# Optimization experiments

Measured on AMD Instinct MI355X. Metric: run time of the kernel, lower is better.

## Reference

```python
import jax, jax.numpy as jnp
import numpy as np

B, C, W, H = 256, 1, 512, 512
D0, D1 = 64, 64            # input_dims: crop/resample target
LATENT = 1024
HIST = 8                   # transformer_history_size (also attention heads)
DEPTH = 4
HEADS = 8
DIM_HEAD = 64              # n_heads arg is used as dim_head
INNER = HEADS * DIM_HEAD   # 512
MLP = LATENT
NCLS = 1000
EPS = 1e-5
RESNET_GAIN = 2.0 ** 7     # 7 identity ResidualBlocks, each does x += x


def setup_inputs() -> dict:
    key = jax.random.key(0)
    ks = jax.random.split(key, 12)
    def rn(k, shape):
        return jax.random.normal(k, shape, jnp.float32) * 0.02
    return dict(
        x=jax.random.normal(ks[0], (B, C, W, H), jnp.float32),
        transformation=jax.random.uniform(ks[1], (B, 4), dtype=jnp.float32),
        history=jnp.zeros((HIST, B, LATENT), jnp.float32),
        w_img=rn(ks[2], (D0 * D1, LATENT)), b_img=jnp.zeros((LATENT,), jnp.float32),
        ln1_s=jnp.ones((DEPTH, LATENT), jnp.float32), ln1_b=jnp.zeros((DEPTH, LATENT), jnp.float32),
        w_qkv=rn(ks[3], (DEPTH, LATENT, 3 * INNER)),
        w_o=rn(ks[4], (DEPTH, INNER, LATENT)), b_o=jnp.zeros((DEPTH, LATENT), jnp.float32),
        ln2_s=jnp.ones((DEPTH, LATENT), jnp.float32), ln2_b=jnp.zeros((DEPTH, LATENT), jnp.float32),
        w_ff1=rn(ks[5], (DEPTH, LATENT, MLP)), b_ff1=jnp.zeros((DEPTH, MLP), jnp.float32),
        w_ff2=rn(ks[6], (DEPTH, MLP, LATENT)), b_ff2=jnp.zeros((DEPTH, LATENT), jnp.float32),
        w_cls=rn(ks[7], (HIST * LATENT, NCLS)), b_cls=jnp.zeros((NCLS,), jnp.float32),
        w_tr=rn(ks[8], (HIST * LATENT, 4)), b_tr=jnp.zeros((4,), jnp.float32),
    )


def _ln(x, s, b):
    m = x.mean(-1, keepdims=True)
    v = x.var(-1, keepdims=True)
    return (x - m) / jnp.sqrt(v + EPS) * s + b


def _crop_one(img, sc):
    # img [C,W,H], sc = [px, py, zx, zy]; nearest crop+resample to (D0, D1)
    px, py, zx, zy = sc[0], sc[1], sc[2], sc[3]
    x1 = px * (W - D0)
    y1 = py * (H - D1)
    xs = jnp.minimum(W - x1, zx * (W - D0) + D0)
    ys = jnp.minimum(H - y1, zy * (H - D1) + D1)
    xi = jnp.clip((jnp.floor(jnp.arange(D0, dtype=jnp.float32) / D0 * xs) + x1).astype(jnp.int32), 0, W - 1)
    yi = jnp.clip((jnp.floor(jnp.arange(D1, dtype=jnp.float32) / D1 * ys) + y1).astype(jnp.int32), 0, H - 1)
    # itertools.product(c, xi, yi) ordering == reshape(-1) of [C, D0, D1]
    return img[:, xi[:, None], yi[None, :]].reshape(-1)


def _forward(x, transformation, history, w_img, b_img, ln1_s, ln1_b, w_qkv, w_o, b_o,
             ln2_s, ln2_b, w_ff1, b_ff1, w_ff2, b_ff2, w_cls, b_cls, w_tr, b_tr):
    crops = jax.vmap(_crop_one)(x, transformation)          # [B, C*D0*D1]
    feats = crops * RESNET_GAIN                             # ResNet18 == scale by 2^7
    image_latent = feats @ w_img + b_img                    # [B, LATENT]
    # history.append(latent); take last HIST; stack dim=1 -> [B, HIST, LATENT]
    hist = jnp.transpose(history, (1, 0, 2))                # [B, HIST, LATENT]
    z = jnp.concatenate([hist[:, 1:], image_latent[:, None, :]], axis=1)
    scale = DIM_HEAD ** -0.5
    for i in range(DEPTH):
        h = _ln(z, ln1_s[i], ln1_b[i])
        qkv = h @ w_qkv[i]                                  # [B, HIST, 3*INNER]
        q, k, v = jnp.split(qkv, 3, axis=-1)
        q = q.reshape(B, HIST, HEADS, DIM_HEAD).transpose(0, 2, 1, 3)
        k = k.reshape(B, HIST, HEADS, DIM_HEAD).transpose(0, 2, 1, 3)
        v = v.reshape(B, HIST, HEADS, DIM_HEAD).transpose(0, 2, 1, 3)
        attn = jax.nn.softmax(jnp.einsum('bhid,bhjd->bhij', q, k) * scale, axis=-1)
        o = jnp.einsum('bhij,bhjd->bhid', attn, v).transpose(0, 2, 1, 3).reshape(B, HIST, INNER)
        z = o @ w_o[i] + b_o[i] + z
        h2 = _ln(z, ln2_s[i], ln2_b[i])
        z = jax.nn.gelu(h2 @ w_ff1[i] + b_ff1[i], approximate=False) @ w_ff2[i] + b_ff2[i] + z
    tl = z.reshape(B, HIST * LATENT)
    class_pred = tl @ w_cls + b_cls                         # [B, NCLS]
    transform_pred = jax.nn.sigmoid(tl @ w_tr + b_tr)       # [B, 4]
    return class_pred, transform_pred


def reference(x, transformation, history, w_img, b_img, ln1_s, ln1_b, w_qkv, w_o, b_o,
              ln2_s, ln2_b, w_ff1, b_ff1, w_ff2, b_ff2, w_cls, b_cls, w_tr, b_tr):
    return _forward(x, transformation, history, w_img, b_img, ln1_s, ln1_b, w_qkv, w_o, b_o,
                    ln2_s, ln2_b, w_ff1, b_ff1, w_ff2, b_ff2, w_cls, b_cls, w_tr, b_tr)
```

## Files before the change

kernel.cpp:

```cpp
#include <hip/hip_runtime.h>
#include <cstdint>
#include <cstddef>

typedef __attribute__((ext_vector_type(8))) __bf16 bf16x8;
typedef __attribute__((ext_vector_type(8))) unsigned short u16x8;
typedef __attribute__((ext_vector_type(4))) float f32x4;
typedef __attribute__((ext_vector_type(4))) unsigned short u16x4;

__device__ __forceinline__ unsigned short f2bf(float f) {
  unsigned int u = __builtin_bit_cast(unsigned int, f);
  u += 0x7fffu + ((u >> 16) & 1u);
  return (unsigned short)(u >> 16);
}
__device__ __forceinline__ float bf2f(unsigned short u) {
  return __builtin_bit_cast(float, ((unsigned int)u) << 16);
}

__device__ void wcast_tile(char* smemc, int bid,
    const float* s_img, const float* s_qkv, const float* s_o,
    const float* s_ff1, const float* s_ff2, const float* s_cls,
    unsigned short* d_img, unsigned short* d_qkv, unsigned short* d_o,
    unsigned short* d_ff1, unsigned short* d_ff2, unsigned short* d_cls) {
  float (*tile)[65] = (float (*)[65])smemc;
  const float* src; unsigned short* dst; int K, N, Npad, rel;
  if (bid < 1024)       { src = s_img; dst = d_img; K = 4096; N = 1024; Npad = 1024; rel = bid; }
  else if (bid < 2560)  { rel = bid - 1024; int l = rel / 384; rel -= l * 384;
                          src = s_qkv + (size_t)l * 1024 * 1536; dst = d_qkv + (size_t)l * 1536 * 1024;
                          K = 1024; N = 1536; Npad = 1536; }
  else if (bid < 3072)  { rel = bid - 2560; int l = rel / 128; rel -= l * 128;
                          src = s_o   + (size_t)l * 512 * 1024;  dst = d_o   + (size_t)l * 1024 * 512;
                          K = 512;  N = 1024; Npad = 1024; }
  else if (bid < 4096)  { rel = bid - 3072; int l = rel / 256; rel -= l * 256;
                          src = s_ff1 + (size_t)l * 1024 * 1024; dst = d_ff1 + (size_t)l * 1024 * 1024;
                          K = 1024; N = 1024; Npad = 1024; }
  else if (bid < 5120)  { rel = bid - 4096; int l = rel / 256; rel -= l * 256;
                          src = s_ff2 + (size_t)l * 1024 * 1024; dst = d_ff2 + (size_t)l * 1024 * 1024;
                          K = 1024; N = 1024; Npad = 1024; }
  else                  { rel = bid - 5120; src = s_cls; dst = d_cls; K = 8192; N = 1000; Npad = 1024; }
  int tilesX = Npad >> 6;
  int nx = rel % tilesX, ky = rel / tilesX;
  int n0 = nx << 6, k0 = ky << 6;
  int t = threadIdx.x;
#pragma unroll
  for (int i = 0; i < 4; ++i) {
    int slot = t + i * 256;
    int kk = slot >> 4, cq = slot & 15;
    int n = n0 + cq * 4;
    float4 v;
    if (n + 3 < N) v = *(const float4*)(src + (size_t)(k0 + kk) * N + n);
    else {
      v.x = v.y = v.z = v.w = 0.0f;
      if (n < N)     v.x = src[(size_t)(k0 + kk) * N + n];
      if (n + 1 < N) v.y = src[(size_t)(k0 + kk) * N + n + 1];
      if (n + 2 < N) v.z = src[(size_t)(k0 + kk) * N + n + 2];
      if (n + 3 < N) v.w = src[(size_t)(k0 + kk) * N + n + 3];
    }
    tile[kk][cq * 4 + 0] = v.x;
    tile[kk][cq * 4 + 1] = v.y;
    tile[kk][cq * 4 + 2] = v.z;
    tile[kk][cq * 4 + 3] = v.w;
  }
  __syncthreads();
#pragma unroll
  for (int i = 0; i < 4; ++i) {
    int slot = t + i * 256;
    int n = slot >> 4, kq = slot & 15;
    u16x4 o;
    o.x = f2bf(tile[kq * 4 + 0][n]);
    o.y = f2bf(tile[kq * 4 + 1][n]);
    o.z = f2bf(tile[kq * 4 + 2][n]);
    o.w = f2bf(tile[kq * 4 + 3][n]);
    *(u16x4*)(dst + (size_t)(n0 + n) * K + k0 + kq * 4) = o;
  }
}

template <int BK, int ITERS>
__device__ __forceinline__ void stage_tile(const unsigned short* __restrict__ g, int ld,
                                           int k0, char* lbase, int tid) {
  constexpr int CH = BK / 8;
#pragma unroll
  for (int it = 0; it < ITERS; ++it) {
    int c = tid + it * 256;
    int r = c / CH;
    int slot = c & (CH - 1);
    int gc = slot ^ (r & (CH - 1));
    const unsigned short* src = g + (size_t)r * ld + (k0 + gc * 8);
    char* dst = lbase + c * 16;
    __builtin_amdgcn_global_load_lds((__attribute__((address_space(1))) void*)src,
                                     (__attribute__((address_space(3))) void*)dst, 16, 0, 0);
  }
}

template <int BK>
__device__ __forceinline__ bf16x8 ld_frag(const char* base, int row, int k8) {
  constexpr int CH = BK / 8;
  int off = row * (BK * 2) + ((k8 ^ (row & (CH - 1))) << 4);
  return *(const bf16x8*)(base + off);
}

template <int TN, int ACT, int OMODE, bool RES, int BK>
__device__ void gemm_tile(char* smem,
    const unsigned short* __restrict__ A, int lda,
    const unsigned short* __restrict__ BT, int ldb, int Kloop,
    const float* __restrict__ bias, const unsigned short* __restrict__ res,
    float* __restrict__ outF, unsigned short* __restrict__ outB,
    int ldC, int Nstore, int m0, int n0, int koff) {
  constexpr int MR = (TN == 64) ? 2 : 4;
  constexpr int ABYTES = 128 * BK * 2;
  constexpr int BUFS = (128 + TN) * BK * 2;
  constexpr int AITERS = BK / 16;
  constexpr int BITERS = TN * BK / 2048;
  const int tid = threadIdx.x;
  const int lane = tid & 63;
  const int wid = tid >> 6;
  const int rowbase = (TN == 64) ? wid * 32 : (wid >> 1) * 64;
  const int colbase = (TN == 64) ? 0 : (wid & 1) * 64;
  const unsigned short* Ag = A + (size_t)m0 * lda + koff;
  const unsigned short* Bg = BT + (size_t)n0 * ldb + koff;
  f32x4 acc[MR][4];
#pragma unroll
  for (int m = 0; m < MR; m++)
#pragma unroll
    for (int n = 0; n < 4; n++) acc[m][n] = 0.f;
  const int nt = Kloop / BK;
  stage_tile<BK, AITERS>(Ag, lda, 0, smem, tid);
  stage_tile<BK, BITERS>(Bg, ldb, 0, smem + ABYTES, tid);
  __syncthreads();
  int cur = 0;
  const int rA = lane & 15, kq = lane >> 4;
  for (int t = 0; t < nt; ++t) {
    if (t + 1 < nt) {
      stage_tile<BK, AITERS>(Ag, lda, (t + 1) * BK, smem + (cur ^ 1) * BUFS, tid);
      stage_tile<BK, BITERS>(Bg, ldb, (t + 1) * BK, smem + (cur ^ 1) * BUFS + ABYTES, tid);
    }
    const char* la = smem + cur * BUFS;
    const char* lb = la + ABYTES;
#pragma unroll
    for (int kk = 0; kk < BK / 32; ++kk) {
      int k8 = kk * 4 + kq;
      bf16x8 af[MR], bfr[4];
#pragma unroll
      for (int m = 0; m < MR; m++) af[m] = ld_frag<BK>(la, rowbase + m * 16 + rA, k8);
#pragma unroll
      for (int n = 0; n < 4; n++) bfr[n] = ld_frag<BK>(lb, colbase + n * 16 + rA, k8);
#pragma unroll
      for (int m = 0; m < MR; m++)
#pragma unroll
        for (int n = 0; n < 4; n++)
          acc[m][n] = __builtin_amdgcn_mfma_f32_16x16x32_bf16(af[m], bfr[n], acc[m][n], 0, 0, 0);
    }
    __syncthreads();
    cur ^= 1;
  }
  const int rb = m0 + rowbase + (kq << 2);
  const int cb = n0 + colbase + rA;
#pragma unroll
  for (int m = 0; m < MR; m++)
#pragma unroll
    for (int n = 0; n < 4; n++) {
      int cg = cb + n * 16;
      if (cg >= Nstore) continue;
      float bv = bias ? bias[cg] : 0.0f;
#pragma unroll
      for (int j = 0; j < 4; j++) {
        int rg = rb + m * 16 + j;
        float v = acc[m][n][j] + bv;
        if (RES) v += bf2f(res[(size_t)rg * ldC + cg]);
        if (ACT == 1) v = 0.5f * v * (1.0f + erff(v * 0.70710678118654752f));
        if (OMODE == 0) {
          outF[(size_t)rg * ldC + cg] = v;
        } else {
          outB[(size_t)rg * ldC + cg] = f2bf(v);
        }
      }
    }
}

#define SLABW 200
__global__ __launch_bounds__(256) void qkvattn(
    const unsigned short* __restrict__ h,
    const unsigned short* __restrict__ BTq,
    unsigned short* __restrict__ obuf) {
  __shared__ __align__(16) char smem[65536];
  const int tid = threadIdx.x, lane = tid & 63, wid = tid >> 6;
  const int p = blockIdx.x;
  const int xslot = p & 7, rem = p >> 3;
  const int hh = rem & 7;
  const int my = xslot + 8 * (rem >> 3);
  const int m0 = my << 6;
  const int wr = wid >> 1, wc = wid & 1;
  const unsigned short* Ag = h + (size_t)m0 * 1024;
  const unsigned short* Bseg0 = BTq + (size_t)(hh * 64) * 1024;
  const unsigned short* Bseg1 = BTq + (size_t)(512 + hh * 64) * 1024;
  const unsigned short* Bseg2 = BTq + (size_t)(1024 + hh * 64) * 1024;
  constexpr int BUFS = 32768;
  f32x4 acc[2][6];
#pragma unroll
  for (int m = 0; m < 2; m++)
#pragma unroll
    for (int n = 0; n < 6; n++) acc[m][n] = 0.f;
  const int rA = lane & 15, kq = lane >> 4;
  stage_tile<64, 2>(Ag, 1024, 0, smem, tid);
  stage_tile<64, 2>(Bseg0, 1024, 0, smem + 8192, tid);
  stage_tile<64, 2>(Bseg1, 1024, 0, smem + 16384, tid);
  stage_tile<64, 2>(Bseg2, 1024, 0, smem + 24576, tid);
  __syncthreads();
  int cur = 0;
  for (int t = 0; t < 16; ++t) {
    if (t + 1 < 16) {
      char* nb = smem + (cur ^ 1) * BUFS;
      stage_tile<64, 2>(Ag, 1024, (t + 1) << 6, nb, tid);
      stage_tile<64, 2>(Bseg0, 1024, (t + 1) << 6, nb + 8192, tid);
      stage_tile<64, 2>(Bseg1, 1024, (t + 1) << 6, nb + 16384, tid);
      stage_tile<64, 2>(Bseg2, 1024, (t + 1) << 6, nb + 24576, tid);
    }
    const char* la = smem + cur * BUFS;
#pragma unroll
    for (int kk = 0; kk < 2; ++kk) {
      int k8 = kk * 4 + kq;
      bf16x8 af[2], bfr[6];
#pragma unroll
      for (int m = 0; m < 2; m++) af[m] = ld_frag<64>(la, wr * 32 + m * 16 + rA, k8);
#pragma unroll
      for (int n = 0; n < 6; n++) {
        int cidx = wc * 96 + n * 16 + rA;
        bfr[n] = ld_frag<64>(la + 8192 + (cidx >> 6) * 8192, cidx & 63, k8);
      }
#pragma unroll
      for (int m = 0; m < 2; m++)
#pragma unroll
        for (int n = 0; n < 6; n++)
          acc[m][n] = __builtin_amdgcn_mfma_f32_16x16x32_bf16(af[m], bfr[n], acc[m][n], 0, 0, 0);
    }
    __syncthreads();
    cur ^= 1;
  }
  unsigned short* slab = (unsigned short*)smem;
  float* Sb = (float*)(smem + 64 * SLABW * 2 + wid * 512);
#pragma unroll
  for (int m = 0; m < 2; m++)
#pragma unroll
    for (int n = 0; n < 6; n++) {
      int r = wr * 32 + m * 16 + (kq << 2);
      int c = wc * 96 + n * 16 + rA;
#pragma unroll
      for (int j = 0; j < 4; j++) slab[(size_t)(r + j) * SLABW + c] = f2bf(acc[m][n][j]);
    }
  __syncthreads();
  {
#pragma unroll
    for (int e = 0; e < 2; ++e) {
      int idx = e * 64 + lane;
      int bl = idx >> 6;
      int i = (idx >> 3) & 7, j = idx & 7;
      int rb8 = wid * 16 + bl * 8;
      const u16x8* qrow = (const u16x8*)(slab + (size_t)(rb8 + i) * SLABW);
      const u16x8* krow = (const u16x8*)(slab + (size_t)(rb8 + j) * SLABW + 64);
      float s = 0.f;
#pragma unroll
      for (int q8 = 0; q8 < 8; ++q8) {
        u16x8 qv = qrow[q8], kv = krow[q8];
#pragma unroll
        for (int u = 0; u < 8; ++u) s = fmaf(bf2f(qv[u]), bf2f(kv[u]), s);
      }
      Sb[bl * 64 + i * 8 + j] = s * 0.125f;
    }
    if (lane < 16) {
      float4 r0 = ((const float4*)(Sb + lane * 8))[0];
      float4 r1 = ((const float4*)(Sb + lane * 8))[1];
      float mx = fmaxf(fmaxf(fmaxf(r0.x, r0.y), fmaxf(r0.z, r0.w)),
                       fmaxf(fmaxf(r1.x, r1.y), fmaxf(r1.z, r1.w)));
      float e0 = expf(r0.x - mx), e1 = expf(r0.y - mx), e2 = expf(r0.z - mx), e3 = expf(r0.w - mx);
      float e4_ = expf(r1.x - mx), e5 = expf(r1.y - mx), e6 = expf(r1.z - mx), e7 = expf(r1.w - mx);
      float inv = 1.0f / (e0 + e1 + e2 + e3 + e4_ + e5 + e6 + e7);
      ((float4*)(Sb + lane * 8))[0] = make_float4(e0 * inv, e1 * inv, e2 * inv, e3 * inv);
      ((float4*)(Sb + lane * 8))[1] = make_float4(e4_ * inv, e5 * inv, e6 * inv, e7 * inv);
    }
#pragma unroll
    for (int bl = 0; bl < 2; ++bl) {
      int rb8 = wid * 16 + bl * 8;
      float vreg[8];
#pragma unroll
      for (int jj = 0; jj < 8; ++jj) vreg[jj] = bf2f(slab[(size_t)(rb8 + jj) * SLABW + 128 + lane]);
      int browg = (my * 8 + wid * 2 + bl) * 8;
#pragma unroll
      for (int i = 0; i < 8; ++i) {
        float4 p0 = ((const float4*)(Sb + (bl * 64 + i * 8)))[0];
        float4 p1 = ((const float4*)(Sb + (bl * 64 + i * 8)))[1];
        float o = p0.x * vreg[0] + p0.y * vreg[1] + p0.z * vreg[2] + p0.w * vreg[3] +
                  p1.x * vreg[4] + p1.y * vreg[5] + p1.z * vreg[6] + p1.w * vreg[7];
        obuf[(size_t)(browg + i) * 512 + hh * 64 + lane] = f2bf(o);
      }
    }
  }
}

__global__ __launch_bounds__(256) void front1(
    const float* __restrict__ x, const float* __restrict__ tr,
    const float* __restrict__ w_img, const float* __restrict__ w_qkv, const float* __restrict__ w_o,
    const float* __restrict__ w_ff1, const float* __restrict__ w_ff2, const float* __restrict__ w_cls,
    unsigned short* BT_img, unsigned short* BT_qkv, unsigned short* BT_o,
    unsigned short* BT_ff1, unsigned short* BT_ff2, unsigned short* BT_cls,
    unsigned short* feats) {
  __shared__ __align__(16) char smem[16640];
  int bid = blockIdx.x;
  int tid = threadIdx.x;
  if (bid < 1024) {
    wcast_tile(smem, bid, w_img, w_qkv, w_o, w_ff1, w_ff2, w_cls,
               BT_img, BT_qkv, BT_o, BT_ff1, BT_ff2, BT_cls);
  } else {
    int b = bid - 1024;
    int* xi = (int*)smem;
    int* yi = xi + 64;
    float px = tr[b * 4 + 0], py = tr[b * 4 + 1], zx = tr[b * 4 + 2], zy = tr[b * 4 + 3];
    float x1 = __fmul_rn(px, 448.0f);
    float y1 = __fmul_rn(py, 448.0f);
    float xs = fminf(__fsub_rn(512.0f, x1), __fadd_rn(__fmul_rn(zx, 448.0f), 64.0f));
    float ys = fminf(__fsub_rn(512.0f, y1), __fadd_rn(__fmul_rn(zy, 448.0f), 64.0f));
    if (tid < 64) {
      float u = __fmul_rn(__fmul_rn((float)tid, 0.015625f), xs);
      int v = (int)(__fadd_rn(floorf(u), x1));
      xi[tid] = min(max(v, 0), 511);
    } else if (tid < 128) {
      int tt = tid - 64;
      float u = __fmul_rn(__fmul_rn((float)tt, 0.015625f), ys);
      int v = (int)(__fadd_rn(floorf(u), y1));
      yi[tt] = min(max(v, 0), 511);
    }
    __syncthreads();
    const float* img = x + (size_t)b * 262144;
    for (int p = tid; p < 4096; p += 256) {
      int i = p >> 6, j = p & 63;
      float val = img[xi[i] * 512 + yi[j]] * 128.0f;
      feats[(size_t)b * 4096 + p] = f2bf(val);
    }
  }
}

__global__ __launch_bounds__(256) void k_img(
    const unsigned short* __restrict__ feats, const unsigned short* __restrict__ BT_img,
    float* __restrict__ part, const float* __restrict__ hist, unsigned short* __restrict__ z,
    const float* __restrict__ w_img, const float* __restrict__ w_qkv, const float* __restrict__ w_o,
    const float* __restrict__ w_ff1, const float* __restrict__ w_ff2, const float* __restrict__ w_cls,
    unsigned short* BT_img_d, unsigned short* BT_qkv, unsigned short* BT_o,
    unsigned short* BT_ff1, unsigned short* BT_ff2, unsigned short* BT_cls) {
  __shared__ __align__(16) char smem[49152];
  int bid = blockIdx.x;
  if (bid < 256) {
    int xslot = bid & 7, rem = bid >> 3;
    int nx = rem & 15, chi = rem >> 4;
    int c = xslot + 8 * chi;
    int sk = c >> 1, my = c & 1;
    gemm_tile<64, 0, 0, false, 64>(smem, feats, 4096, BT_img, 4096, 512,
                                   nullptr, nullptr, part + (size_t)sk * 262144, nullptr,
                                   1024, 1024, my * 128, nx * 64, sk * 512);
  } else if (bid < 6400) {
    wcast_tile(smem, 1024 + bid - 256, w_img, w_qkv, w_o, w_ff1, w_ff2, w_cls,
               BT_img_d, BT_qkv, BT_o, BT_ff1, BT_ff2, BT_cls);
  } else {
    int idx = (bid - 6400) * 256 + threadIdx.x;
    int off = idx * 4;
    int b = off / 7168;
    int r = off - b * 7168;
    int i = r >> 10, c = r & 1023;
    float4 v = *(const float4*)(hist + (size_t)(i + 1) * 262144 + (size_t)b * 1024 + c);
    u16x4 o;
    o.x = f2bf(v.x); o.y = f2bf(v.y); o.z = f2bf(v.z); o.w = f2bf(v.w);
    *(u16x4*)(z + (size_t)b * 8192 + i * 1024 + c) = o;
  }
}

__device__ __forceinline__ void ln_row(const unsigned short* __restrict__ z, int row,
                                       const float* __restrict__ sc, const float* __restrict__ bi,
                                       unsigned short* __restrict__ h) {
  int lane = threadIdx.x & 63;
  const unsigned short* zr = z + (size_t)row * 1024;
  float vf[16];
  float s = 0.f, q = 0.f;
#pragma unroll
  for (int i = 0; i < 2; i++) {
    u16x8 v = *(const u16x8*)(zr + lane * 8 + i * 512);
#pragma unroll
    for (int u = 0; u < 8; u++) {
      float f = bf2f(v[u]);
      vf[i * 8 + u] = f;
      s += f; q += f * f;
    }
  }
#pragma unroll
  for (int off = 32; off; off >>= 1) { s += __shfl_xor(s, off); q += __shfl_xor(q, off); }
  float mean = s * (1.0f / 1024.0f);
  float var = q * (1.0f / 1024.0f) - mean * mean;
  float rstd = rsqrtf(var + 1e-5f);
#pragma unroll
  for (int i = 0; i < 2; i++) {
    int c = lane * 8 + i * 512;
    float4 s0 = *(const float4*)(sc + c);
    float4 s1 = *(const float4*)(sc + c + 4);
    float4 b0 = *(const float4*)(bi + c);
    float4 b1 = *(const float4*)(bi + c + 4);
    u16x8 o;
    o[0] = f2bf((vf[i * 8 + 0] - mean) * rstd * s0.x + b0.x);
    o[1] = f2bf((vf[i * 8 + 1] - mean) * rstd * s0.y + b0.y);
    o[2] = f2bf((vf[i * 8 + 2] - mean) * rstd * s0.z + b0.z);
    o[3] = f2bf((vf[i * 8 + 3] - mean) * rstd * s0.w + b0.w);
    o[4] = f2bf((vf[i * 8 + 4] - mean) * rstd * s1.x + b1.x);
    o[5] = f2bf((vf[i * 8 + 5] - mean) * rstd * s1.y + b1.y);
    o[6] = f2bf((vf[i * 8 + 6] - mean) * rstd * s1.z + b1.z);
    o[7] = f2bf((vf[i * 8 + 7] - mean) * rstd * s1.w + b1.w);
    *(u16x8*)(h + (size_t)row * 1024 + c) = o;
  }
}

__global__ __launch_bounds__(256) void imgred_ln(
    const float* __restrict__ part, const float* __restrict__ b_img,
    unsigned short* __restrict__ z,
    const float* __restrict__ sc, const float* __restrict__ bi,
    unsigned short* __restrict__ h) {
  __shared__ float ws[8];
  int m = blockIdx.x, tid = threadIdx.x;
  int lane = tid & 63, wid = tid >> 6;
  int c = tid * 4;
  float4 a = {0.f, 0.f, 0.f, 0.f};
  for (int p = 0; p < 8; ++p) {
    float4 v = *(const float4*)(part + (size_t)p * 262144 + m * 1024 + c);
    a.x += v.x; a.y += v.y; a.z += v.z; a.w += v.w;
  }
  float4 bv = *(const float4*)(b_img + c);
  a.x += bv.x; a.y += bv.y; a.z += bv.z; a.w += bv.w;
  u16x4 zo;
  zo.x = f2bf(a.x); zo.y = f2bf(a.y); zo.z = f2bf(a.z); zo.w = f2bf(a.w);
  *(u16x4*)(z + (size_t)m * 8192 + 7168 + c) = zo;
  float s = a.x + a.y + a.z + a.w;
  float q = a.x * a.x + a.y * a.y + a.z * a.z + a.w * a.w;
#pragma unroll
  for (int off = 32; off; off >>= 1) { s += __shfl_xor(s, off); q += __shfl_xor(q, off); }
  if (lane == 0) { ws[wid * 2] = s; ws[wid * 2 + 1] = q; }
  __syncthreads();
  float S4 = ws[0] + ws[2] + ws[4] + ws[6];
  float Q4 = ws[1] + ws[3] + ws[5] + ws[7];
  float mean = S4 * (1.0f / 1024.0f);
  float var = Q4 * (1.0f / 1024.0f) - mean * mean;
  float rstd = rsqrtf(var + 1e-5f);
  float4 sv = *(const float4*)(sc + c);
  float4 bb = *(const float4*)(bi + c);
  u16x4 o;
  o.x = f2bf((a.x - mean) * rstd * sv.x + bb.x);
  o.y = f2bf((a.y - mean) * rstd * sv.y + bb.y);
  o.z = f2bf((a.z - mean) * rstd * sv.z + bb.z);
  o.w = f2bf((a.w - mean) * rstd * sv.w + bb.w);
  *(u16x4*)(h + (size_t)(m * 8 + 7) * 1024 + c) = o;
#pragma unroll
  for (int rr = 0; rr < 2; ++rr) {
    int r = wid * 2 + rr;
    if (r < 7) ln_row(z, m * 8 + r, sc, bi, h);
  }
}

__global__ __launch_bounds__(256) void ln_kernel(const unsigned short* __restrict__ z,
                                                 const float* __restrict__ sc,
                                                 const float* __restrict__ bi,
                                                 unsigned short* __restrict__ h) {
  int row = blockIdx.x * 4 + (threadIdx.x >> 6);
  ln_row(z, row, sc, bi, h);
}

template <int TN, int ACT, int OMODE, bool RES, int BK>
__global__ __launch_bounds__(256) void gemm_k(
    const unsigned short* __restrict__ A, int lda,
    const unsigned short* __restrict__ BT, int ldb, int Kloop,
    const float* __restrict__ bias, const unsigned short* __restrict__ res,
    float* __restrict__ outF, unsigned short* __restrict__ outB,
    int ldC, int Nstore) {
  constexpr int BUFS = (128 + TN) * BK * 2;
  __shared__ __align__(16) char smem[2 * BUFS];
  int p = blockIdx.x;
  int xslot = p & 7, rem = p >> 3;
  int nx = rem & 15;
  int my = xslot + 8 * (rem >> 4);
  gemm_tile<TN, ACT, OMODE, RES, BK>(smem, A, lda, BT, ldb, Kloop, bias, res, outF, outB,
                                     ldC, Nstore, my * 128, nx * TN, 0);
}

__global__ __launch_bounds__(256) void k_cls(
    const unsigned short* __restrict__ z, const unsigned short* __restrict__ BT_cls,
    float* __restrict__ part, const float* __restrict__ w_tr,
    const float* __restrict__ b_tr, float* __restrict__ outF) {
  __shared__ __align__(16) char smem[49152];
  int bid = blockIdx.x;
  int tid = threadIdx.x;
  if (bid < 256) {
    int xslot = bid & 7, rem = bid >> 3;
    int nx = rem & 15, chi = rem >> 4;
    int c = xslot + 8 * chi;
    int sk = c >> 1, my = c & 1;
    gemm_tile<64, 0, 0, false, 64>(smem, z, 8192, BT_cls, 8192, 1024,
                                   nullptr, nullptr, part + (size_t)sk * 262144, nullptr,
                                   1024, 1024, my * 128, nx * 64, sk * 1024);
  } else {
    int m = bid - 256;
    const unsigned short* row = z + (size_t)m * 8192;
    float a0 = 0.f, a1 = 0.f, a2 = 0.f, a3 = 0.f;
    for (int k = tid; k < 8192; k += 256) {
      float xv = bf2f(row[k]);
      const float* wr = w_tr + (size_t)k * 4;
      a0 += xv * wr[0]; a1 += xv * wr[1]; a2 += xv * wr[2]; a3 += xv * wr[3];
    }
    float (*red)[4] = (float (*)[4])smem;
    red[tid][0] = a0; red[tid][1] = a1; red[tid][2] = a2; red[tid][3] = a3;
    __syncthreads();
    for (int s = 128; s > 0; s >>= 1) {
      if (tid < s) {
#pragma unroll
        for (int o = 0; o < 4; o++) red[tid][o] += red[tid + s][o];
      }
      __syncthreads();
    }
    if (tid < 4) {
      float v = red[0][tid] + b_tr[tid];
      outF[256000 + m * 4 + tid] = 1.0f / (1.0f + expf(-v));
    }
  }
}

__global__ __launch_bounds__(256) void clsred(const float* __restrict__ part,
                                              const float* __restrict__ b_cls,
                                              float* __restrict__ outF) {
  int m = blockIdx.x, c = threadIdx.x * 4;
  float4 a = {0.f, 0.f, 0.f, 0.f};
  for (int p = 0; p < 8; ++p) {
    float4 v = *(const float4*)(part + (size_t)p * 262144 + m * 1024 + c);
    a.x += v.x; a.y += v.y; a.z += v.z; a.w += v.w;
  }
  if (c >= 1000) return;
  float* drow = outF + (size_t)m * 1000;
  float vals[4] = {a.x, a.y, a.z, a.w};
  if (c + 3 < 1000) {
    *(float4*)(drow + c) = make_float4(vals[0] + b_cls[c], vals[1] + b_cls[c + 1],
                                       vals[2] + b_cls[c + 2], vals[3] + b_cls[c + 3]);
  } else {
    for (int j = 0; j < 4 && c + j < 1000; ++j) drow[c + j] = vals[j] + b_cls[c + j];
  }
}

extern "C" void kernel_launch(void* const* d_in, const int* in_sizes, int n_in,
                              void* d_out, int out_size, void* d_ws, size_t ws_size,
                              hipStream_t stream) {
  const float* x      = (const float*)d_in[0];
  const float* tr     = (const float*)d_in[1];
  const float* hist   = (const float*)d_in[2];
  const float* w_img  = (const float*)d_in[3];
  const float* b_img  = (const float*)d_in[4];
  const float* ln1_s  = (const float*)d_in[5];
  const float* ln1_b  = (const float*)d_in[6];
  const float* w_qkv  = (const float*)d_in[7];
  const float* w_o    = (const float*)d_in[8];
  const float* b_o    = (const float*)d_in[9];
  const float* ln2_s  = (const float*)d_in[10];
  const float* ln2_b  = (const float*)d_in[11];
  const float* w_ff1  = (const float*)d_in[12];
  const float* b_ff1  = (const float*)d_in[13];
  const float* w_ff2  = (const float*)d_in[14];
  const float* b_ff2  = (const float*)d_in[15];
  const float* w_cls  = (const float*)d_in[16];
  const float* b_cls  = (const float*)d_in[17];
  const float* w_tr   = (const float*)d_in[18];
  const float* b_tr   = (const float*)d_in[19];
  float* outF = (float*)d_out;

  char* w = (char*)d_ws;
  auto alloc = [&](size_t bytes) { char* p = w; w += (bytes + 255) & ~(size_t)255; return p; };
  unsigned short* BT_img = (unsigned short*)alloc((size_t)1024 * 4096 * 2);
  unsigned short* BT_qkv = (unsigned short*)alloc((size_t)4 * 1536 * 1024 * 2);
  unsigned short* BT_o   = (unsigned short*)alloc((size_t)4 * 1024 * 512 * 2);
  unsigned short* BT_ff1 = (unsigned short*)alloc((size_t)4 * 1024 * 1024 * 2);
  unsigned short* BT_ff2 = (unsigned short*)alloc((size_t)4 * 1024 * 1024 * 2);
  unsigned short* BT_cls = (unsigned short*)alloc((size_t)1024 * 8192 * 2);
  unsigned short* feats  = (unsigned short*)alloc((size_t)256 * 4096 * 2);
  unsigned short* z      = (unsigned short*)alloc((size_t)2048 * 1024 * 2);
  unsigned short* h      = (unsigned short*)alloc((size_t)2048 * 1024 * 2);
  unsigned short* obuf   = (unsigned short*)alloc((size_t)2048 * 512 * 2);
  unsigned short* g      = (unsigned short*)alloc((size_t)2048 * 1024 * 2);
  float*          part   = (float*)alloc((size_t)8 * 256 * 1024 * 4);
  if ((size_t)(w - (char*)d_ws) > ws_size) return;

  front1<<<1280, 256, 0, stream>>>(x, tr, w_img, w_qkv, w_o, w_ff1, w_ff2, w_cls,
                                   BT_img, BT_qkv, BT_o, BT_ff1, BT_ff2, BT_cls, feats);
  k_img<<<8192, 256, 0, stream>>>(feats, BT_img, part, hist, z,
                                  w_img, w_qkv, w_o, w_ff1, w_ff2, w_cls,
                                  BT_img, BT_qkv, BT_o, BT_ff1, BT_ff2, BT_cls);
  imgred_ln<<<256, 256, 0, stream>>>(part, b_img, z, ln1_s, ln1_b, h);

  for (int i = 0; i < 4; ++i) {
    const unsigned short* Wq = BT_qkv + (size_t)i * 1536 * 1024;
    const unsigned short* Wo = BT_o   + (size_t)i * 1024 * 512;
    const unsigned short* W1 = BT_ff1 + (size_t)i * 1024 * 1024;
    const unsigned short* W2 = BT_ff2 + (size_t)i * 1024 * 1024;
    if (i > 0)
      ln_kernel<<<512, 256, 0, stream>>>(z, ln1_s + i * 1024, ln1_b + i * 1024, h);
    qkvattn<<<256, 256, 0, stream>>>(h, Wq, obuf);
    gemm_k<64, 0, 1, true, 64><<<256, 256, 0, stream>>>(
        obuf, 512, Wo, 512, 512, b_o + i * 1024, z, nullptr, z, 1024, 1024);
    ln_kernel<<<512, 256, 0, stream>>>(z, ln2_s + i * 1024, ln2_b + i * 1024, h);
    gemm_k<64, 1, 1, false, 64><<<256, 256, 0, stream>>>(
        h, 1024, W1, 1024, 1024, b_ff1 + i * 1024, nullptr, nullptr, g, 1024, 1024);
    gemm_k<64, 0, 1, true, 64><<<256, 256, 0, stream>>>(
        g, 1024, W2, 1024, 1024, b_ff2 + i * 1024, z, nullptr, z, 1024, 1024);
  }

  k_cls<<<512, 256, 0, stream>>>(z, BT_cls, part, w_tr, b_tr, outF);
  clsred<<<256, 256, 0, stream>>>(part, b_cls, outF);
}
```

Measured before the change: 323.1 us.

## Triple-buffer GEMM LDS staging with explicit vmcnt waits instead of full syncs

Converts the double-buffered async global-to-LDS pipeline in the shared GEMM tile and the fused QKV-attention kernel to a three-stage ring. Each iteration waits on vmcnt only until the oldest stage has landed and uses one raw barrier, where before it drained all loads with __syncthreads. Loads are issued two tiles ahead so memory latency can hide behind more MFMA work. In exchange LDS per block grows by half, which may reduce occupancy, and correctness depends on the hand-set vmcnt thresholds matching the number of issued loads.

```diff
diff --git a/kernel.cpp b/kernel.cpp
--- a/kernel.cpp
+++ b/kernel.cpp
@@ -14,6 +14,13 @@
 }
 __device__ __forceinline__ float bf2f(unsigned short u) {
   return __builtin_bit_cast(float, ((unsigned int)u) << 16);
+}
+
+template <int N> __device__ __forceinline__ void wait_vm() {
+  if constexpr (N == 0)      asm volatile("s_waitcnt vmcnt(0)" ::: "memory");
+  else if constexpr (N == 6) asm volatile("s_waitcnt vmcnt(6)" ::: "memory");
+  else if constexpr (N == 8) asm volatile("s_waitcnt vmcnt(8)" ::: "memory");
+  else                       asm volatile("s_waitcnt vmcnt(0)" ::: "memory");
 }
 
 __device__ void wcast_tile(char* smemc, int bid,
@@ -72,6 +79,7 @@
     o.w = f2bf(tile[kq * 4 + 3][n]);
     *(u16x4*)(dst + (size_t)(n0 + n) * K + k0 + kq * 4) = o;
   }
+  __syncthreads();
 }
 
 template <int BK, int ITERS>
@@ -110,6 +118,7 @@
   constexpr int BUFS = (128 + TN) * BK * 2;
   constexpr int AITERS = BK / 16;
   constexpr int BITERS = TN * BK / 2048;
+  constexpr int VM = AITERS + BITERS;
   const int tid = threadIdx.x;
   const int lane = tid & 63;
   const int wid = tid >> 6;
@@ -125,13 +134,17 @@
   const int nt = Kloop / BK;
   stage_tile<BK, AITERS>(Ag, lda, 0, smem, tid);
   stage_tile<BK, BITERS>(Bg, ldb, 0, smem + ABYTES, tid);
-  __syncthreads();
+  stage_tile<BK, AITERS>(Ag, lda, BK, smem + BUFS, tid);
+  stage_tile<BK, BITERS>(Bg, ldb, BK, smem + BUFS + ABYTES, tid);
   int cur = 0;
   const int rA = lane & 15, kq = lane >> 4;
   for (int t = 0; t < nt; ++t) {
-    if (t + 1 < nt) {
-      stage_tile<BK, AITERS>(Ag, lda, (t + 1) * BK, smem + (cur ^ 1) * BUFS, tid);
-      stage_tile<BK, BITERS>(Bg, ldb, (t + 1) * BK, smem + (cur ^ 1) * BUFS + ABYTES, tid);
+    if (t + 1 < nt) wait_vm<VM>(); else wait_vm<0>();
+    __builtin_amdgcn_s_barrier();
+    if (t + 2 < nt) {
+      int nb = cur + 2; if (nb >= 3) nb -= 3;
+      stage_tile<BK, AITERS>(Ag, lda, (t + 2) * BK, smem + nb * BUFS, tid);
+      stage_tile<BK, BITERS>(Bg, ldb, (t + 2) * BK, smem + nb * BUFS + ABYTES, tid);
     }
     const char* la = smem + cur * BUFS;
     const char* lb = la + ABYTES;
@@ -149,8 +162,7 @@
         for (int n = 0; n < 4; n++)
           acc[m][n] = __builtin_amdgcn_mfma_f32_16x16x32_bf16(af[m], bfr[n], acc[m][n], 0, 0, 0);
     }
-    __syncthreads();
-    cur ^= 1;
+    cur = (cur + 1 == 3) ? 0 : cur + 1;
   }
   const int rb = m0 + rowbase + (kq << 2);
   const int cb = n0 + colbase + rA;
@@ -181,7 +193,7 @@
     const unsigned short* __restrict__ h,
     const unsigned short* __restrict__ BTq,
     unsigned short* __restrict__ obuf) {
-  __shared__ __align__(16) char smem[65536];
+  __shared__ __align__(16) char smem[98304];
   const int tid = threadIdx.x, lane = tid & 63, wid = tid >> 6;
   const int p = blockIdx.x;
   const int xslot = p & 7, rem = p >> 3;
@@ -200,19 +212,25 @@
 #pragma unroll
     for (int n = 0; n < 6; n++) acc[m][n] = 0.f;
   const int rA = lane & 15, kq = lane >> 4;
-  stage_tile<64, 2>(Ag, 1024, 0, smem, tid);
-  stage_tile<64, 2>(Bseg0, 1024, 0, smem + 8192, tid);
-  stage_tile<64, 2>(Bseg1, 1024, 0, smem + 16384, tid);
-  stage_tile<64, 2>(Bseg2, 1024, 0, smem + 24576, tid);
-  __syncthreads();
+#pragma unroll
+  for (int pt = 0; pt < 2; ++pt) {
+    char* b = smem + pt * BUFS;
+    stage_tile<64, 2>(Ag, 1024, pt * 64, b, tid);
+    stage_tile<64, 2>(Bseg0, 1024, pt * 64, b + 8192, tid);
+    stage_tile<64, 2>(Bseg1, 1024, pt * 64, b + 16384, tid);
+    stage_tile<64, 2>(Bseg2, 1024, pt * 64, b + 24576, tid);
+  }
   int cur = 0;
   for (int t = 0; t < 16; ++t) {
-    if (t + 1 < 16) {
-      char* nb = smem + (cur ^ 1) * BUFS;
-      stage_tile<64, 2>(Ag, 1024, (t + 1) << 6, nb, tid);
-      stage_tile<64, 2>(Bseg0, 1024, (t + 1) << 6, nb + 8192, tid);
-      stage_tile<64, 2>(Bseg1, 1024, (t + 1) << 6, nb + 16384, tid);
-      stage_tile<64, 2>(Bseg2, 1024, (t + 1) << 6, nb + 24576, tid);
+    if (t + 1 < 16) wait_vm<8>(); else wait_vm<0>();
+    __builtin_amdgcn_s_barrier();
+    if (t + 2 < 16) {
+      int nbid = cur + 2; if (nbid >= 3) nbid -= 3;
+      char* nb = smem + nbid * BUFS;
+      stage_tile<64, 2>(Ag, 1024, (t + 2) << 6, nb, tid);
+      stage_tile<64, 2>(Bseg0, 1024, (t + 2) << 6, nb + 8192, tid);
+      stage_tile<64, 2>(Bseg1, 1024, (t + 2) << 6, nb + 16384, tid);
+      stage_tile<64, 2>(Bseg2, 1024, (t + 2) << 6, nb + 24576, tid);
     }
     const char* la = smem + cur * BUFS;
 #pragma unroll
@@ -232,9 +250,9 @@
         for (int n = 0; n < 6; n++)
           acc[m][n] = __builtin_amdgcn_mfma_f32_16x16x32_bf16(af[m], bfr[n], acc[m][n], 0, 0, 0);
     }
-    __syncthreads();
-    cur ^= 1;
-  }
+    cur = (cur + 1 == 3) ? 0 : cur + 1;
+  }
+  __syncthreads();
   unsigned short* slab = (unsigned short*)smem;
   float* Sb = (float*)(smem + 64 * SLABW * 2 + wid * 512);
 #pragma unroll
@@ -344,7 +362,7 @@
     const float* __restrict__ w_ff1, const float* __restrict__ w_ff2, const float* __restrict__ w_cls,
     unsigned short* BT_img_d, unsigned short* BT_qkv, unsigned short* BT_o,
     unsigned short* BT_ff1, unsigned short* BT_ff2, unsigned short* BT_cls) {
-  __shared__ __align__(16) char smem[49152];
+  __shared__ __align__(16) char smem[73728];
   int bid = blockIdx.x;
   if (bid < 256) {
     int xslot = bid & 7, rem = bid >> 3;
@@ -473,7 +491,7 @@
     float* __restrict__ outF, unsigned short* __restrict__ outB,
     int ldC, int Nstore) {
   constexpr int BUFS = (128 + TN) * BK * 2;
-  __shared__ __align__(16) char smem[2 * BUFS];
+  __shared__ __align__(16) char smem[3 * BUFS];
   int p = blockIdx.x;
   int xslot = p & 7, rem = p >> 3;
   int nx = rem & 15;
@@ -486,7 +504,7 @@
     const unsigned short* __restrict__ z, const unsigned short* __restrict__ BT_cls,
     float* __restrict__ part, const float* __restrict__ w_tr,
     const float* __restrict__ b_tr, float* __restrict__ outF) {
-  __shared__ __align__(16) char smem[49152];
+  __shared__ __align__(16) char smem[73728];
   int bid = blockIdx.x;
   int tid = threadIdx.x;
   if (bid < 256) {
```

Result: faster. 293.4 us, median of 2 (-9.2%).
